# Kernel tuning notes

Measured on AMD Instinct MI355X. Metric: run time of the kernel, lower is better.

## Reference

```python
import jax, jax.numpy as jnp
import numpy as np

B, S, D = 4, 2048, 1024  # batch, seq_len, model dim (= qk_dim = output_dim)


def setup_inputs() -> dict:
    key = jax.random.key(0)
    kq, kk, kv, kwq, kwk, kwv = jax.random.split(key, 6)
    q = jax.random.normal(kq, (B, S, D), dtype=jnp.float32)
    k = jax.random.normal(kk, (B, S, D), dtype=jnp.float32)
    v = jax.random.normal(kv, (B, S, D), dtype=jnp.float32)
    # causal mask, broadcast over batch
    mask = jnp.broadcast_to(jnp.tril(jnp.ones((S, S), dtype=bool)), (B, S, S))
    W_q = jax.random.uniform(kwq, (D, D), dtype=jnp.float32)
    W_k = jax.random.uniform(kwk, (D, D), dtype=jnp.float32)
    W_v = jax.random.uniform(kwv, (D, D), dtype=jnp.float32)
    return {"q": q, "k": k, "v": v, "mask": mask, "W_q": W_q, "W_k": W_k, "W_v": W_v}


def reference(q, k, v, mask, W_q, W_k, W_v):
    q1 = q @ W_q  # (B, S, D)
    k1 = k @ W_k  # (B, S, D)
    v1 = v @ W_v  # (B, S, D)
    qk = jnp.einsum('bij,bkj->bik', q1, k1)  # (B, S, S)
    qk = qk * jax.lax.rsqrt(float(k1.shape[-1]))
    neg_inf = jnp.finfo(jnp.float32).min
    qk = jnp.where(mask, qk, neg_inf)
    s = jax.nn.softmax(qk, axis=-1)
    return jnp.einsum('bij,bjk->bik', s, v1)
```

## Files before the change

### kernel.cpp

```cpp
#include <hip/hip_runtime.h>
#include <hip/hip_bf16.h>
#include <float.h>


typedef __attribute__((ext_vector_type(8))) short bf16x8;
typedef __attribute__((ext_vector_type(4))) float f32x4;

#define MFMA16 __builtin_amdgcn_mfma_f32_16x16x32_bf16

union U8 { bf16x8 v; unsigned w[4]; };

__device__ __forceinline__ ushort f2bf(float x) {
  union { float f; unsigned u; } v; v.f = x;
  unsigned r = v.u + 0x7fffu + ((v.u >> 16) & 1u);
  return (ushort)(r >> 16);
}
__device__ __forceinline__ float bf2f(ushort h) {
  union { unsigned u; float f; } v; v.u = ((unsigned)h) << 16;
  return v.f;
}
__device__ __forceinline__ void splitf(float x, ushort& hi, ushort& lo) {
  hi = f2bf(x);
  lo = f2bf(x - bf2f(hi));
}

__device__ __forceinline__ bf16x8 cvt8(const float* lp) {
  U8 H;
#pragma unroll
  for (int p = 0; p < 4; ++p) {
    const unsigned u0 = __float_as_uint(lp[2 * p]);
    const unsigned u1 = __float_as_uint(lp[2 * p + 1]);
    const unsigned r0 = (u0 + 0x7fffu + ((u0 >> 16) & 1u)) >> 16;
    const unsigned r1 = (u1 + 0x7fffu + ((u1 >> 16) & 1u)) & 0xffff0000u;
    H.w[p] = r0 | r1;
  }
  return H.v;
}

#define GLOAD16(gp, lp)                                                        \
  __builtin_amdgcn_global_load_lds(                                            \
      (const __attribute__((address_space(1))) void*)(gp),                     \
      (__attribute__((address_space(3))) void*)(lp), 16, 0, 0)

__device__ __forceinline__ void stage_bf16_32(const ushort* g, int pitch,
                                              ushort* lds, int w, int lane) {
#pragma unroll
  for (int i = 0; i < 2; ++i) {
    const int c = w * 2 + i;
    const int row = c * 16 + (lane >> 2);
    const int kp = (lane & 3) * 8;
    GLOAD16(g + (size_t)row * pitch + kp, lds + c * 512);
  }
}
__device__ __forceinline__ void stage_bf16_64(const ushort* g, int pitch,
                                              ushort* lds, int w, int lane) {
#pragma unroll
  for (int i = 0; i < 4; ++i) {
    const int c = w * 4 + i;
    const int row = c * 8 + (lane >> 3);
    const int kp = (lane & 7) * 8;
    GLOAD16(g + (size_t)row * pitch + kp, lds + c * 512);
  }
}
__device__ __forceinline__ void stage_f32_32(const float* g, int pitch,
                                             float* lds, int w, int lane) {
#pragma unroll
  for (int i = 0; i < 4; ++i) {
    const int c = w * 4 + i;
    const int row = c * 8 + (lane >> 3);
    const int kp = (lane & 7) * 4;
    GLOAD16(g + (size_t)row * pitch + kp, lds + c * 256);
  }
}

__global__ __launch_bounds__(256) void split_pre(
    const float* __restrict__ q, const float* __restrict__ k,
    ushort* __restrict__ qh, ushort* __restrict__ ql,
    ushort* __restrict__ kh, ushort* __restrict__ kl) {
  const float* X = blockIdx.y ? k : q;
  ushort* H = blockIdx.y ? kh : qh;
  ushort* L = blockIdx.y ? kl : ql;
  const int n4 = 2097152;
  for (int i = blockIdx.x * 256 + threadIdx.x; i < n4; i += 2048 * 256) {
    const float4 x = reinterpret_cast<const float4*>(X)[i];
    ushort h0, l0, h1, l1, h2, l2, h3, l3;
    splitf(x.x, h0, l0); splitf(x.y, h1, l1);
    splitf(x.z, h2, l2); splitf(x.w, h3, l3);
    reinterpret_cast<ushort4*>(H)[i] = ushort4{h0, h1, h2, h3};
    reinterpret_cast<ushort4*>(L)[i] = ushort4{l0, l1, l2, l3};
  }
}

__global__ __launch_bounds__(256) void wt_conv(
    const float* __restrict__ W0, const float* __restrict__ W1,
    const float* __restrict__ W2, ushort* __restrict__ Th0,
    ushort* __restrict__ Tl0, ushort* __restrict__ Th1,
    ushort* __restrict__ Tl1, ushort* __restrict__ Th2) {
  __shared__ float t[32][33];
  const int z = blockIdx.z;
  const float* W = z == 0 ? W0 : (z == 1 ? W1 : W2);
  ushort* Th = z == 0 ? Th0 : (z == 1 ? Th1 : Th2);
  ushort* Tl = z == 0 ? Tl0 : (z == 1 ? Tl1 : nullptr);
  const int bx = blockIdx.x, by = blockIdx.y;
  const int r = threadIdx.x >> 3, c4 = (threadIdx.x & 7) * 4;
  const float4 x =
      *reinterpret_cast<const float4*>(&W[(size_t)(bx * 32 + r) * 1024 + by * 32 + c4]);
  t[r][c4] = x.x; t[r][c4 + 1] = x.y; t[r][c4 + 2] = x.z; t[r][c4 + 3] = x.w;
  __syncthreads();
  ushort h[4], l[4];
#pragma unroll
  for (int j = 0; j < 4; ++j) splitf(t[c4 + j][r], h[j], l[j]);
  const size_t o = (size_t)(by * 32 + r) * 1024 + bx * 32 + c4;
  *reinterpret_cast<ushort4*>(&Th[o]) = ushort4{h[0], h[1], h[2], h[3]};
  if (Tl)
    *reinterpret_cast<ushort4*>(&Tl[o]) = ushort4{l[0], l[1], l[2], l[3]};
}

__global__ __launch_bounds__(256) void proj_qk(
    const ushort* __restrict__ Ah0, const ushort* __restrict__ Al0,
    const ushort* __restrict__ Ah1, const ushort* __restrict__ Al1,
    const ushort* __restrict__ Bh0, const ushort* __restrict__ Bl0,
    const ushort* __restrict__ Bh1, const ushort* __restrict__ Bl1,
    ushort* __restrict__ Oh0, ushort* __restrict__ Ol0,
    ushort* __restrict__ Oh1, ushort* __restrict__ Ol1) {
  __shared__ ushort Ahs[4096], Als[4096], Bhs[4096], Bls[4096];
  const int f = blockIdx.x;
  const int xb = (f >> 3) & 7;
  const int r = (f & 7) + ((f >> 6) << 3);
  const int yb = r & 63, z = r >> 6;
  const ushort* Ah = z ? Ah1 : Ah0;
  const ushort* Al = z ? Al1 : Al0;
  const ushort* Bh = z ? Bh1 : Bh0;
  const ushort* Bl = z ? Bl1 : Bl0;
  ushort* Oh = z ? Oh1 : Oh0;
  ushort* Ol = z ? Ol1 : Ol0;
  const int tid = threadIdx.x, lane = tid & 63, w = tid >> 6;
  const int wr = w >> 1, wc = w & 1;
  const int lr = lane & 15, kg = lane >> 4;
  const int m0 = yb * 128, n0 = xb * 128;
  f32x4 acc[4][4] = {};

  for (int k0 = 0; k0 < 1024; k0 += 32) {
    stage_bf16_32(Ah + (size_t)m0 * 1024 + k0, 1024, Ahs, w, lane);
    stage_bf16_32(Al + (size_t)m0 * 1024 + k0, 1024, Als, w, lane);
    stage_bf16_32(Bh + (size_t)n0 * 1024 + k0, 1024, Bhs, w, lane);
    stage_bf16_32(Bl + (size_t)n0 * 1024 + k0, 1024, Bls, w, lane);
    __syncthreads();
    bf16x8 ah[4], al[4], bh[4], bl[4];
#pragma unroll
    for (int m = 0; m < 4; ++m) {
      ah[m] = *reinterpret_cast<bf16x8*>(&Ahs[(wr * 64 + m * 16 + lr) * 32 + kg * 8]);
      al[m] = *reinterpret_cast<bf16x8*>(&Als[(wr * 64 + m * 16 + lr) * 32 + kg * 8]);
    }
#pragma unroll
    for (int n = 0; n < 4; ++n) {
      bh[n] = *reinterpret_cast<bf16x8*>(&Bhs[(wc * 64 + n * 16 + lr) * 32 + kg * 8]);
      bl[n] = *reinterpret_cast<bf16x8*>(&Bls[(wc * 64 + n * 16 + lr) * 32 + kg * 8]);
    }
#pragma unroll
    for (int m = 0; m < 4; ++m)
#pragma unroll
      for (int n = 0; n < 4; ++n) {
        acc[m][n] = MFMA16(ah[m], bh[n], acc[m][n], 0, 0, 0);
        acc[m][n] = MFMA16(ah[m], bl[n], acc[m][n], 0, 0, 0);
        acc[m][n] = MFMA16(al[m], bh[n], acc[m][n], 0, 0, 0);
      }
    __syncthreads();
  }
#pragma unroll
  for (int m = 0; m < 4; ++m)
#pragma unroll
    for (int n = 0; n < 4; ++n)
#pragma unroll
      for (int reg = 0; reg < 4; ++reg) {
        const int gm = m0 + wr * 64 + m * 16 + kg * 4 + reg;
        const int gn = n0 + wc * 64 + n * 16 + lr;
        ushort h, l;
        splitf(acc[m][n][reg], h, l);
        Oh[(size_t)gm * 1024 + gn] = h;
        Ol[(size_t)gm * 1024 + gn] = l;
      }
}

__global__ __launch_bounds__(256) void proj_v(const ushort* __restrict__ Wvt,
                                              const float* __restrict__ V,
                                              ushort* __restrict__ v1t) {
  __shared__ ushort Ahs[4096];
  __shared__ float Bs[4096];
  const int f = blockIdx.x;
  const int yb = (f >> 3) & 7;
  const int xb = (f & 7) + ((f >> 6) << 3);
  const int tid = threadIdx.x, lane = tid & 63, w = tid >> 6;
  const int wr = w >> 1, wc = w & 1;
  const int lr = lane & 15, kg = lane >> 4;
  const int m0 = yb * 128;
  const int n0 = xb * 128;
  f32x4 acc[4][4] = {};

  for (int k0 = 0; k0 < 1024; k0 += 32) {
    stage_bf16_32(Wvt + (size_t)m0 * 1024 + k0, 1024, Ahs, w, lane);
    stage_f32_32(V + (size_t)n0 * 1024 + k0, 1024, Bs, w, lane);
    __syncthreads();
    bf16x8 ah[4], bh[4];
#pragma unroll
    for (int m = 0; m < 4; ++m)
      ah[m] = *reinterpret_cast<bf16x8*>(&Ahs[(wr * 64 + m * 16 + lr) * 32 + kg * 8]);
#pragma unroll
    for (int n = 0; n < 4; ++n)
      bh[n] = cvt8(&Bs[(wc * 64 + n * 16 + lr) * 32 + kg * 8]);
#pragma unroll
    for (int m = 0; m < 4; ++m)
#pragma unroll
      for (int n = 0; n < 4; ++n)
        acc[m][n] = MFMA16(ah[m], bh[n], acc[m][n], 0, 0, 0);
    __syncthreads();
  }
#pragma unroll
  for (int m = 0; m < 4; ++m)
#pragma unroll
    for (int n = 0; n < 4; ++n)
#pragma unroll
      for (int reg = 0; reg < 4; ++reg) {
        const int gm = m0 + wr * 64 + m * 16 + kg * 4 + reg;
        const int gn = n0 + wc * 64 + n * 16 + lr;
        const int b = gn >> 11, jj = gn & 2047;
        v1t[((size_t)b << 21) + (size_t)gm * 2048 + jj] = f2bf(acc[m][n][reg]);
      }
}

__global__ __launch_bounds__(256) void qk2(
    const ushort* __restrict__ q1h, const ushort* __restrict__ q1l,
    const ushort* __restrict__ k1h, const ushort* __restrict__ k1l,
    float* __restrict__ scoresA, float* __restrict__ scoresB) {
  __shared__ ushort Ahs[4096], Als[4096], Bhs[4096], Bls[4096];
  const int f = blockIdx.x;
  const int s = (f & 7) * 136 + (f >> 3);
  const int z = s / 544;
  const int rem = s % 544;
  const int b = rem / 136;
  int p = rem % 136, ti = 0, accp = 0;
  while (accp + ti + 1 <= p) { accp += ti + 1; ++ti; }
  const int tj = p - accp;
  const int tid = threadIdx.x, lane = tid & 63, w = tid >> 6;
  const int wr = w >> 1, wc = w & 1;
  const int lr = lane & 15, kg = lane >> 4;
  const int kh0 = z * 512;
  const ushort* qh = q1h + ((size_t)b * 2048 + ti * 128) * 1024 + kh0;
  const ushort* ql = q1l + ((size_t)b * 2048 + ti * 128) * 1024 + kh0;
  const ushort* kh = k1h + ((size_t)b * 2048 + tj * 128) * 1024 + kh0;
  const ushort* kl = k1l + ((size_t)b * 2048 + tj * 128) * 1024 + kh0;
  f32x4 acc[4][4] = {};

  for (int k0 = 0; k0 < 512; k0 += 32) {
    stage_bf16_32(qh + k0, 1024, Ahs, w, lane);
    stage_bf16_32(ql + k0, 1024, Als, w, lane);
    stage_bf16_32(kh + k0, 1024, Bhs, w, lane);
    stage_bf16_32(kl + k0, 1024, Bls, w, lane);
    __syncthreads();
    bf16x8 ah[4], al[4], bh[4], bl[4];
#pragma unroll
    for (int m = 0; m < 4; ++m) {
      ah[m] = *reinterpret_cast<bf16x8*>(&Ahs[(wr * 64 + m * 16 + lr) * 32 + kg * 8]);
      al[m] = *reinterpret_cast<bf16x8*>(&Als[(wr * 64 + m * 16 + lr) * 32 + kg * 8]);
    }
#pragma unroll
    for (int n = 0; n < 4; ++n) {
      bh[n] = *reinterpret_cast<bf16x8*>(&Bhs[(wc * 64 + n * 16 + lr) * 32 + kg * 8]);
      bl[n] = *reinterpret_cast<bf16x8*>(&Bls[(wc * 64 + n * 16 + lr) * 32 + kg * 8]);
    }
#pragma unroll
    for (int m = 0; m < 4; ++m)
#pragma unroll
      for (int n = 0; n < 4; ++n) {
        acc[m][n] = MFMA16(ah[m], bh[n], acc[m][n], 0, 0, 0);
        acc[m][n] = MFMA16(ah[m], bl[n], acc[m][n], 0, 0, 0);
        acc[m][n] = MFMA16(al[m], bh[n], acc[m][n], 0, 0, 0);
      }
    __syncthreads();
  }
  const float sc = 0.03125f;
  float* st = (z ? scoresB : scoresA) + ((size_t)b * 136 + p) * 16384;
#pragma unroll
  for (int m = 0; m < 4; ++m)
#pragma unroll
    for (int n = 0; n < 4; ++n)
#pragma unroll
      for (int reg = 0; reg < 4; ++reg) {
        const int il = wr * 64 + m * 16 + kg * 4 + reg;
        const int jl = wc * 64 + n * 16 + lr;
        st[il * 128 + jl] = acc[m][n][reg] * sc;
      }
}

__global__ __launch_bounds__(256) void softmax_kernel(
    float* __restrict__ scoresA, const float* __restrict__ scoresB) {
  __shared__ float red[8];
  const int rb = blockIdx.x;
  const int b = rb >> 11, r = rb & 2047;
  const int ti = r >> 7, rl = r & 127, ncol = (ti + 1) * 128;
  const int valid = r + 1;
  const size_t tbase = ((size_t)b * 136 + (ti * (ti + 1)) / 2) * 16384;
  float* srowA = scoresA + tbase;
  const float* srowB = scoresB + tbase;
  const int tid = threadIdx.x, lane = tid & 63, w = tid >> 6;

  float vals[2][4];
  float mx = -FLT_MAX;
#pragma unroll
  for (int c = 0; c < 2; ++c) {
    const int j = tid * 4 + c * 1024;
    const size_t o = (size_t)(j >> 7) * 16384 + rl * 128 + (j & 127);
    const float4 a = *reinterpret_cast<const float4*>(srowA + o);
    const float4 bb = *reinterpret_cast<const float4*>(srowB + o);
    vals[c][0] = (j + 0 < valid) ? a.x + bb.x : -FLT_MAX;
    vals[c][1] = (j + 1 < valid) ? a.y + bb.y : -FLT_MAX;
    vals[c][2] = (j + 2 < valid) ? a.z + bb.z : -FLT_MAX;
    vals[c][3] = (j + 3 < valid) ? a.w + bb.w : -FLT_MAX;
    mx = fmaxf(mx, fmaxf(fmaxf(vals[c][0], vals[c][1]),
                         fmaxf(vals[c][2], vals[c][3])));
  }
#pragma unroll
  for (int o = 32; o; o >>= 1) mx = fmaxf(mx, __shfl_xor(mx, o));
  if (lane == 0) red[w] = mx;
  __syncthreads();
  mx = fmaxf(fmaxf(red[0], red[1]), fmaxf(red[2], red[3]));

  float ex[2][4];
  float sum = 0.f;
#pragma unroll
  for (int c = 0; c < 2; ++c)
#pragma unroll
    for (int e = 0; e < 4; ++e) {
      const int j = tid * 4 + c * 1024 + e;
      ex[c][e] = (j < valid) ? __expf(vals[c][e] - mx) : 0.f;
      sum += ex[c][e];
    }
#pragma unroll
  for (int o = 32; o; o >>= 1) sum += __shfl_xor(sum, o);
  if (lane == 0) red[4 + w] = sum;
  __syncthreads();
  sum = red[4] + red[5] + red[6] + red[7];
  const float inv = 1.f / sum;
#pragma unroll
  for (int c = 0; c < 2; ++c) {
    const int j = tid * 4 + c * 1024;
    if (j < ncol) {
      ushort* pt = reinterpret_cast<ushort*>(srowA + (size_t)(j >> 7) * 16384);
      ushort4 pw;
      pw.x = f2bf(ex[c][0] * inv); pw.y = f2bf(ex[c][1] * inv);
      pw.z = f2bf(ex[c][2] * inv); pw.w = f2bf(ex[c][3] * inv);
      *reinterpret_cast<ushort4*>(&pt[rl * 256 + (j & 127)]) = pw;
    }
  }
}

__global__ __launch_bounds__(256) void pv2(const float* __restrict__ scores,
                                           const ushort* __restrict__ v1t,
                                           float* __restrict__ out) {
  __shared__ ushort Ps[128 * 64], Vs[128 * 64];
  const int fl = blockIdx.x;
  const int s = (fl & 7) * 64 + (fl >> 3);
  const int xb = s & 7, yb = (s >> 3) & 15, b = s >> 7;
  const int tid = threadIdx.x, lane = tid & 63, w = tid >> 6;
  const int wr = w >> 1, wc = w & 1;
  const int lr = lane & 15, kg = lane >> 4;
  const int ti = 15 - yb;
  const int n0 = xb * 128;
  const int tri_ti = (ti * (ti + 1)) / 2;
  const ushort* vbase = v1t + ((size_t)b << 21) + (size_t)n0 * 2048;
  const int kend = (ti + 1) * 128;
  f32x4 acc[4][4] = {};

  for (int k0 = 0; k0 < kend; k0 += 64) {
    const ushort* pt = reinterpret_cast<const ushort*>(
        scores + ((size_t)b * 136 + tri_ti + (k0 >> 7)) * 16384);
    stage_bf16_64(pt + (k0 & 64), 256, Ps, w, lane);
    stage_bf16_64(vbase + k0, 2048, Vs, w, lane);
    __syncthreads();
#pragma unroll
    for (int t2 = 0; t2 < 2; ++t2) {
      bf16x8 pa[4], vb[4];
#pragma unroll
      for (int m = 0; m < 4; ++m)
        pa[m] = *reinterpret_cast<bf16x8*>(
            &Ps[(wr * 64 + m * 16 + lr) * 64 + t2 * 32 + kg * 8]);
#pragma unroll
      for (int n = 0; n < 4; ++n)
        vb[n] = *reinterpret_cast<bf16x8*>(
            &Vs[(wc * 64 + n * 16 + lr) * 64 + t2 * 32 + kg * 8]);
#pragma unroll
      for (int m = 0; m < 4; ++m)
#pragma unroll
        for (int n = 0; n < 4; ++n)
          acc[m][n] = MFMA16(pa[m], vb[n], acc[m][n], 0, 0, 0);
    }
    __syncthreads();
  }
#pragma unroll
  for (int m = 0; m < 4; ++m)
#pragma unroll
    for (int n = 0; n < 4; ++n)
#pragma unroll
      for (int reg = 0; reg < 4; ++reg) {
        const int gm = ti * 128 + wr * 64 + m * 16 + kg * 4 + reg;
        const int gn = n0 + wc * 64 + n * 16 + lr;
        out[((size_t)b * 2048 + gm) * 1024 + gn] = acc[m][n][reg];
      }
}

extern "C" void kernel_launch(void* const* d_in, const int* in_sizes, int n_in,
                              void* d_out, int out_size, void* d_ws,
                              size_t ws_size, hipStream_t stream) {
  const float* q = (const float*)d_in[0];
  const float* k = (const float*)d_in[1];
  const float* v = (const float*)d_in[2];
  const float* Wq = (const float*)d_in[4];
  const float* Wk = (const float*)d_in[5];
  const float* Wv = (const float*)d_in[6];
  float* out = (float*)d_out;

  char* ws = (char*)d_ws;
  const size_t SCORES_T = 35651584;
  float* scoresA = (float*)ws;
  float* scoresB = (float*)(ws + SCORES_T);
  ushort* qsh = (ushort*)ws;
  ushort* qsl = qsh + 8388608;
  ushort* ksh = qsh + 2 * 8388608;
  ushort* ksl = qsh + 3 * 8388608;
  ushort* q1hi = (ushort*)(ws + 2 * SCORES_T);
  ushort* q1lo = q1hi + 8388608;
  ushort* k1hi = q1hi + 2 * 8388608;
  ushort* k1lo = q1hi + 3 * 8388608;
  ushort* v1t = (ushort*)(ws + 2 * SCORES_T);
  ushort* Wqth = (ushort*)(ws + 2 * SCORES_T + 67108864);
  ushort* Wqtl = Wqth + 1048576;
  ushort* Wkth = Wqth + 2097152;
  ushort* Wktl = Wqth + 3145728;
  ushort* Wvt  = Wqth + 4194304;
  const size_t need = 2 * SCORES_T + 67108864 + 10485760;
  if (ws_size < need) return;

  dim3 blk(256);
  wt_conv<<<dim3(32, 32, 3), blk, 0, stream>>>(Wq, Wk, Wv, Wqth, Wqtl, Wkth,
                                               Wktl, Wvt);
  split_pre<<<dim3(2048, 2), blk, 0, stream>>>(q, k, qsh, qsl, ksh, ksl);
  proj_qk<<<dim3(1024), blk, 0, stream>>>(qsh, qsl, ksh, ksl, Wqth, Wqtl,
                                          Wkth, Wktl, q1hi, q1lo, k1hi, k1lo);
  qk2<<<dim3(1088), blk, 0, stream>>>(q1hi, q1lo, k1hi, k1lo, scoresA,
                                      scoresB);
  softmax_kernel<<<dim3(8192), blk, 0, stream>>>(scoresA, scoresB);
  proj_v<<<dim3(512), blk, 0, stream>>>(Wvt, v, v1t);
  pv2<<<dim3(512), blk, 0, stream>>>(scoresA, v1t, out);
}
```

Before: 314.9 us.

## Merge independent launches into combined kernels and halve PV tile width

Weight transpose/split and the q/k split now run as branches of one kernel, and softmax and the V projection share one launch selected by block index. This removes two launches and lets independent work overlap on the GPU. The PV kernel now uses 128x64 output tiles instead of 128x128, doubling the block count to 1024 for better load balance over the causal triangle, at the cost of reloading the P tiles twice as often. Softmax blocks are now launched in the same grid as the MFMA-heavy projection blocks and must share shared-memory sizing with them, which can lower softmax occupancy.

```diff
diff --git a/kernel.cpp b/kernel.cpp
--- a/kernel.cpp
+++ b/kernel.cpp
@@ -62,6 +62,16 @@
     GLOAD16(g + (size_t)row * pitch + kp, lds + c * 512);
   }
 }
+__device__ __forceinline__ void stage_bf16_64x64(const ushort* g, int pitch,
+                                                 ushort* lds, int w, int lane) {
+#pragma unroll
+  for (int i = 0; i < 2; ++i) {
+    const int c = w * 2 + i;
+    const int row = c * 8 + (lane >> 3);
+    const int kp = (lane & 7) * 8;
+    GLOAD16(g + (size_t)row * pitch + kp, lds + c * 512);
+  }
+}
 __device__ __forceinline__ void stage_f32_32(const float* g, int pitch,
                                              float* lds, int w, int lane) {
 #pragma unroll
@@ -73,47 +83,49 @@
   }
 }
 
-__global__ __launch_bounds__(256) void split_pre(
+__global__ __launch_bounds__(256) void wt_split(
     const float* __restrict__ q, const float* __restrict__ k,
-    ushort* __restrict__ qh, ushort* __restrict__ ql,
-    ushort* __restrict__ kh, ushort* __restrict__ kl) {
-  const float* X = blockIdx.y ? k : q;
-  ushort* H = blockIdx.y ? kh : qh;
-  ushort* L = blockIdx.y ? kl : ql;
-  const int n4 = 2097152;
-  for (int i = blockIdx.x * 256 + threadIdx.x; i < n4; i += 2048 * 256) {
-    const float4 x = reinterpret_cast<const float4*>(X)[i];
-    ushort h0, l0, h1, l1, h2, l2, h3, l3;
-    splitf(x.x, h0, l0); splitf(x.y, h1, l1);
-    splitf(x.z, h2, l2); splitf(x.w, h3, l3);
-    reinterpret_cast<ushort4*>(H)[i] = ushort4{h0, h1, h2, h3};
-    reinterpret_cast<ushort4*>(L)[i] = ushort4{l0, l1, l2, l3};
-  }
-}
-
-__global__ __launch_bounds__(256) void wt_conv(
     const float* __restrict__ W0, const float* __restrict__ W1,
     const float* __restrict__ W2, ushort* __restrict__ Th0,
     ushort* __restrict__ Tl0, ushort* __restrict__ Th1,
-    ushort* __restrict__ Tl1, ushort* __restrict__ Th2) {
+    ushort* __restrict__ Tl1, ushort* __restrict__ Th2,
+    ushort* __restrict__ qh, ushort* __restrict__ ql,
+    ushort* __restrict__ kh, ushort* __restrict__ kl) {
   __shared__ float t[32][33];
-  const int z = blockIdx.z;
-  const float* W = z == 0 ? W0 : (z == 1 ? W1 : W2);
-  ushort* Th = z == 0 ? Th0 : (z == 1 ? Th1 : Th2);
-  ushort* Tl = z == 0 ? Tl0 : (z == 1 ? Tl1 : nullptr);
-  const int bx = blockIdx.x, by = blockIdx.y;
-  const int r = threadIdx.x >> 3, c4 = (threadIdx.x & 7) * 4;
-  const float4 x =
-      *reinterpret_cast<const float4*>(&W[(size_t)(bx * 32 + r) * 1024 + by * 32 + c4]);
-  t[r][c4] = x.x; t[r][c4 + 1] = x.y; t[r][c4 + 2] = x.z; t[r][c4 + 3] = x.w;
-  __syncthreads();
-  ushort h[4], l[4];
-#pragma unroll
-  for (int j = 0; j < 4; ++j) splitf(t[c4 + j][r], h[j], l[j]);
-  const size_t o = (size_t)(by * 32 + r) * 1024 + bx * 32 + c4;
-  *reinterpret_cast<ushort4*>(&Th[o]) = ushort4{h[0], h[1], h[2], h[3]};
-  if (Tl)
-    *reinterpret_cast<ushort4*>(&Tl[o]) = ushort4{l[0], l[1], l[2], l[3]};
+  const int f = blockIdx.x;
+  if (f < 3072) {
+    const int z = f >> 10, r10 = f & 1023;
+    const int bx = r10 & 31, by = r10 >> 5;
+    const float* W = z == 0 ? W0 : (z == 1 ? W1 : W2);
+    ushort* Th = z == 0 ? Th0 : (z == 1 ? Th1 : Th2);
+    ushort* Tl = z == 0 ? Tl0 : (z == 1 ? Tl1 : nullptr);
+    const int r = threadIdx.x >> 3, c4 = (threadIdx.x & 7) * 4;
+    const float4 x = *reinterpret_cast<const float4*>(
+        &W[(size_t)(bx * 32 + r) * 1024 + by * 32 + c4]);
+    t[r][c4] = x.x; t[r][c4 + 1] = x.y; t[r][c4 + 2] = x.z; t[r][c4 + 3] = x.w;
+    __syncthreads();
+    ushort h[4], l[4];
+#pragma unroll
+    for (int j = 0; j < 4; ++j) splitf(t[c4 + j][r], h[j], l[j]);
+    const size_t o = (size_t)(by * 32 + r) * 1024 + bx * 32 + c4;
+    *reinterpret_cast<ushort4*>(&Th[o]) = ushort4{h[0], h[1], h[2], h[3]};
+    if (Tl)
+      *reinterpret_cast<ushort4*>(&Tl[o]) = ushort4{l[0], l[1], l[2], l[3]};
+  } else {
+    const int fl = f - 3072;
+    const float* X = (fl >> 11) ? k : q;
+    ushort* H = (fl >> 11) ? kh : qh;
+    ushort* L = (fl >> 11) ? kl : ql;
+    const int n4 = 2097152;
+    for (int i = (fl & 2047) * 256 + threadIdx.x; i < n4; i += 2048 * 256) {
+      const float4 x = reinterpret_cast<const float4*>(X)[i];
+      ushort h0, l0, h1, l1, h2, l2, h3, l3;
+      splitf(x.x, h0, l0); splitf(x.y, h1, l1);
+      splitf(x.z, h2, l2); splitf(x.w, h3, l3);
+      reinterpret_cast<ushort4*>(H)[i] = ushort4{h0, h1, h2, h3};
+      reinterpret_cast<ushort4*>(L)[i] = ushort4{l0, l1, l2, l3};
+    }
+  }
 }
 
 __global__ __launch_bounds__(256) void proj_qk(
@@ -182,52 +194,6 @@
       }
 }
 
-__global__ __launch_bounds__(256) void proj_v(const ushort* __restrict__ Wvt,
-                                              const float* __restrict__ V,
-                                              ushort* __restrict__ v1t) {
-  __shared__ ushort Ahs[4096];
-  __shared__ float Bs[4096];
-  const int f = blockIdx.x;
-  const int yb = (f >> 3) & 7;
-  const int xb = (f & 7) + ((f >> 6) << 3);
-  const int tid = threadIdx.x, lane = tid & 63, w = tid >> 6;
-  const int wr = w >> 1, wc = w & 1;
-  const int lr = lane & 15, kg = lane >> 4;
-  const int m0 = yb * 128;
-  const int n0 = xb * 128;
-  f32x4 acc[4][4] = {};
-
-  for (int k0 = 0; k0 < 1024; k0 += 32) {
-    stage_bf16_32(Wvt + (size_t)m0 * 1024 + k0, 1024, Ahs, w, lane);
-    stage_f32_32(V + (size_t)n0 * 1024 + k0, 1024, Bs, w, lane);
-    __syncthreads();
-    bf16x8 ah[4], bh[4];
-#pragma unroll
-    for (int m = 0; m < 4; ++m)
-      ah[m] = *reinterpret_cast<bf16x8*>(&Ahs[(wr * 64 + m * 16 + lr) * 32 + kg * 8]);
-#pragma unroll
-    for (int n = 0; n < 4; ++n)
-      bh[n] = cvt8(&Bs[(wc * 64 + n * 16 + lr) * 32 + kg * 8]);
-#pragma unroll
-    for (int m = 0; m < 4; ++m)
-#pragma unroll
-      for (int n = 0; n < 4; ++n)
-        acc[m][n] = MFMA16(ah[m], bh[n], acc[m][n], 0, 0, 0);
-    __syncthreads();
-  }
-#pragma unroll
-  for (int m = 0; m < 4; ++m)
-#pragma unroll
-    for (int n = 0; n < 4; ++n)
-#pragma unroll
-      for (int reg = 0; reg < 4; ++reg) {
-        const int gm = m0 + wr * 64 + m * 16 + kg * 4 + reg;
-        const int gn = n0 + wc * 64 + n * 16 + lr;
-        const int b = gn >> 11, jj = gn & 2047;
-        v1t[((size_t)b << 21) + (size_t)gm * 2048 + jj] = f2bf(acc[m][n][reg]);
-      }
-}
-
 __global__ __launch_bounds__(256) void qk2(
     const ushort* __restrict__ q1h, const ushort* __restrict__ q1l,
     const ushort* __restrict__ k1h, const ushort* __restrict__ k1l,
@@ -292,106 +258,154 @@
       }
 }
 
-__global__ __launch_bounds__(256) void softmax_kernel(
-    float* __restrict__ scoresA, const float* __restrict__ scoresB) {
-  __shared__ float red[8];
-  const int rb = blockIdx.x;
-  const int b = rb >> 11, r = rb & 2047;
-  const int ti = r >> 7, rl = r & 127, ncol = (ti + 1) * 128;
-  const int valid = r + 1;
-  const size_t tbase = ((size_t)b * 136 + (ti * (ti + 1)) / 2) * 16384;
-  float* srowA = scoresA + tbase;
-  const float* srowB = scoresB + tbase;
+__global__ __launch_bounds__(256) void sm_projv(
+    float* __restrict__ scoresA, const float* __restrict__ scoresB,
+    const ushort* __restrict__ Wvt, const float* __restrict__ V,
+    ushort* __restrict__ v1t) {
+  __shared__ __align__(16) char smem[24576];
   const int tid = threadIdx.x, lane = tid & 63, w = tid >> 6;
-
-  float vals[2][4];
-  float mx = -FLT_MAX;
-#pragma unroll
-  for (int c = 0; c < 2; ++c) {
-    const int j = tid * 4 + c * 1024;
-    const size_t o = (size_t)(j >> 7) * 16384 + rl * 128 + (j & 127);
-    const float4 a = *reinterpret_cast<const float4*>(srowA + o);
-    const float4 bb = *reinterpret_cast<const float4*>(srowB + o);
-    vals[c][0] = (j + 0 < valid) ? a.x + bb.x : -FLT_MAX;
-    vals[c][1] = (j + 1 < valid) ? a.y + bb.y : -FLT_MAX;
-    vals[c][2] = (j + 2 < valid) ? a.z + bb.z : -FLT_MAX;
-    vals[c][3] = (j + 3 < valid) ? a.w + bb.w : -FLT_MAX;
-    mx = fmaxf(mx, fmaxf(fmaxf(vals[c][0], vals[c][1]),
-                         fmaxf(vals[c][2], vals[c][3])));
-  }
-#pragma unroll
-  for (int o = 32; o; o >>= 1) mx = fmaxf(mx, __shfl_xor(mx, o));
-  if (lane == 0) red[w] = mx;
-  __syncthreads();
-  mx = fmaxf(fmaxf(red[0], red[1]), fmaxf(red[2], red[3]));
-
-  float ex[2][4];
-  float sum = 0.f;
-#pragma unroll
-  for (int c = 0; c < 2; ++c)
-#pragma unroll
-    for (int e = 0; e < 4; ++e) {
-      const int j = tid * 4 + c * 1024 + e;
-      ex[c][e] = (j < valid) ? __expf(vals[c][e] - mx) : 0.f;
-      sum += ex[c][e];
-    }
-#pragma unroll
-  for (int o = 32; o; o >>= 1) sum += __shfl_xor(sum, o);
-  if (lane == 0) red[4 + w] = sum;
-  __syncthreads();
-  sum = red[4] + red[5] + red[6] + red[7];
-  const float inv = 1.f / sum;
-#pragma unroll
-  for (int c = 0; c < 2; ++c) {
-    const int j = tid * 4 + c * 1024;
-    if (j < ncol) {
-      ushort* pt = reinterpret_cast<ushort*>(srowA + (size_t)(j >> 7) * 16384);
-      ushort4 pw;
-      pw.x = f2bf(ex[c][0] * inv); pw.y = f2bf(ex[c][1] * inv);
-      pw.z = f2bf(ex[c][2] * inv); pw.w = f2bf(ex[c][3] * inv);
-      *reinterpret_cast<ushort4*>(&pt[rl * 256 + (j & 127)]) = pw;
-    }
+  const int fg = blockIdx.x;
+  if (fg < 8192) {
+    float* red = reinterpret_cast<float*>(smem);
+    const int b = fg >> 11, r = fg & 2047;
+    const int ti = r >> 7, rl = r & 127, ncol = (ti + 1) * 128;
+    const int valid = r + 1;
+    const size_t tbase = ((size_t)b * 136 + (ti * (ti + 1)) / 2) * 16384;
+    float* srowA = scoresA + tbase;
+    const float* srowB = scoresB + tbase;
+
+    float vals[2][4];
+    float mx = -FLT_MAX;
+#pragma unroll
+    for (int c = 0; c < 2; ++c) {
+      const int j = tid * 4 + c * 1024;
+      const size_t o = (size_t)(j >> 7) * 16384 + rl * 128 + (j & 127);
+      const float4 a = *reinterpret_cast<const float4*>(srowA + o);
+      const float4 bb = *reinterpret_cast<const float4*>(srowB + o);
+      vals[c][0] = (j + 0 < valid) ? a.x + bb.x : -FLT_MAX;
+      vals[c][1] = (j + 1 < valid) ? a.y + bb.y : -FLT_MAX;
+      vals[c][2] = (j + 2 < valid) ? a.z + bb.z : -FLT_MAX;
+      vals[c][3] = (j + 3 < valid) ? a.w + bb.w : -FLT_MAX;
+      mx = fmaxf(mx, fmaxf(fmaxf(vals[c][0], vals[c][1]),
+                           fmaxf(vals[c][2], vals[c][3])));
+    }
+#pragma unroll
+    for (int o = 32; o; o >>= 1) mx = fmaxf(mx, __shfl_xor(mx, o));
+    if (lane == 0) red[w] = mx;
+    __syncthreads();
+    mx = fmaxf(fmaxf(red[0], red[1]), fmaxf(red[2], red[3]));
+
+    float ex[2][4];
+    float sum = 0.f;
+#pragma unroll
+    for (int c = 0; c < 2; ++c)
+#pragma unroll
+      for (int e = 0; e < 4; ++e) {
+        const int j = tid * 4 + c * 1024 + e;
+        ex[c][e] = (j < valid) ? __expf(vals[c][e] - mx) : 0.f;
+        sum += ex[c][e];
+      }
+#pragma unroll
+    for (int o = 32; o; o >>= 1) sum += __shfl_xor(sum, o);
+    if (lane == 0) red[4 + w] = sum;
+    __syncthreads();
+    sum = red[4] + red[5] + red[6] + red[7];
+    const float inv = 1.f / sum;
+#pragma unroll
+    for (int c = 0; c < 2; ++c) {
+      const int j = tid * 4 + c * 1024;
+      if (j < ncol) {
+        ushort* pt =
+            reinterpret_cast<ushort*>(srowA + (size_t)(j >> 7) * 16384);
+        ushort4 pw;
+        pw.x = f2bf(ex[c][0] * inv); pw.y = f2bf(ex[c][1] * inv);
+        pw.z = f2bf(ex[c][2] * inv); pw.w = f2bf(ex[c][3] * inv);
+        *reinterpret_cast<ushort4*>(&pt[rl * 256 + (j & 127)]) = pw;
+      }
+    }
+  } else {
+    ushort* Ahs = reinterpret_cast<ushort*>(smem);
+    float* Bs = reinterpret_cast<float*>(smem + 8192);
+    const int f2 = fg - 8192;
+    const int yb = (f2 >> 3) & 7;
+    const int xb = (f2 & 7) + ((f2 >> 6) << 3);
+    const int wr = w >> 1, wc = w & 1;
+    const int lr = lane & 15, kg = lane >> 4;
+    const int m0 = yb * 128;
+    const int n0 = xb * 128;
+    f32x4 acc[4][4] = {};
+
+    for (int k0 = 0; k0 < 1024; k0 += 32) {
+      stage_bf16_32(Wvt + (size_t)m0 * 1024 + k0, 1024, Ahs, w, lane);
+      stage_f32_32(V + (size_t)n0 * 1024 + k0, 1024, Bs, w, lane);
+      __syncthreads();
+      bf16x8 ah[4], bh[4];
+#pragma unroll
+      for (int m = 0; m < 4; ++m)
+        ah[m] = *reinterpret_cast<bf16x8*>(
+            &Ahs[(wr * 64 + m * 16 + lr) * 32 + kg * 8]);
+#pragma unroll
+      for (int n = 0; n < 4; ++n)
+        bh[n] = cvt8(&Bs[(wc * 64 + n * 16 + lr) * 32 + kg * 8]);
+#pragma unroll
+      for (int m = 0; m < 4; ++m)
+#pragma unroll
+        for (int n = 0; n < 4; ++n)
+          acc[m][n] = MFMA16(ah[m], bh[n], acc[m][n], 0, 0, 0);
+      __syncthreads();
+    }
+#pragma unroll
+    for (int m = 0; m < 4; ++m)
+#pragma unroll
+      for (int n = 0; n < 4; ++n)
+#pragma unroll
+        for (int reg = 0; reg < 4; ++reg) {
+          const int gm = m0 + wr * 64 + m * 16 + kg * 4 + reg;
+          const int gn = n0 + wc * 64 + n * 16 + lr;
+          const int b = gn >> 11, jj = gn & 2047;
+          v1t[((size_t)b << 21) + (size_t)gm * 2048 + jj] = f2bf(acc[m][n][reg]);
+        }
   }
 }
 
 __global__ __launch_bounds__(256) void pv2(const float* __restrict__ scores,
                                            const ushort* __restrict__ v1t,
                                            float* __restrict__ out) {
-  __shared__ ushort Ps[128 * 64], Vs[128 * 64];
+  __shared__ ushort Ps[128 * 64], Vs[64 * 64];
   const int fl = blockIdx.x;
-  const int s = (fl & 7) * 64 + (fl >> 3);
-  const int xb = s & 7, yb = (s >> 3) & 15, b = s >> 7;
+  const int s = (fl & 7) * 128 + (fl >> 3);
+  const int b = s >> 8, rem = s & 255;
+  const int ti = 15 - (rem >> 4);
+  const int n0 = (rem & 15) * 64;
   const int tid = threadIdx.x, lane = tid & 63, w = tid >> 6;
   const int wr = w >> 1, wc = w & 1;
   const int lr = lane & 15, kg = lane >> 4;
-  const int ti = 15 - yb;
-  const int n0 = xb * 128;
   const int tri_ti = (ti * (ti + 1)) / 2;
   const ushort* vbase = v1t + ((size_t)b << 21) + (size_t)n0 * 2048;
   const int kend = (ti + 1) * 128;
-  f32x4 acc[4][4] = {};
+  f32x4 acc[4][2] = {};
 
   for (int k0 = 0; k0 < kend; k0 += 64) {
     const ushort* pt = reinterpret_cast<const ushort*>(
         scores + ((size_t)b * 136 + tri_ti + (k0 >> 7)) * 16384);
     stage_bf16_64(pt + (k0 & 64), 256, Ps, w, lane);
-    stage_bf16_64(vbase + k0, 2048, Vs, w, lane);
+    stage_bf16_64x64(vbase + k0, 2048, Vs, w, lane);
     __syncthreads();
 #pragma unroll
     for (int t2 = 0; t2 < 2; ++t2) {
-      bf16x8 pa[4], vb[4];
+      bf16x8 pa[4], vb[2];
 #pragma unroll
       for (int m = 0; m < 4; ++m)
         pa[m] = *reinterpret_cast<bf16x8*>(
             &Ps[(wr * 64 + m * 16 + lr) * 64 + t2 * 32 + kg * 8]);
 #pragma unroll
-      for (int n = 0; n < 4; ++n)
+      for (int n = 0; n < 2; ++n)
         vb[n] = *reinterpret_cast<bf16x8*>(
-            &Vs[(wc * 64 + n * 16 + lr) * 64 + t2 * 32 + kg * 8]);
+            &Vs[(wc * 32 + n * 16 + lr) * 64 + t2 * 32 + kg * 8]);
 #pragma unroll
       for (int m = 0; m < 4; ++m)
 #pragma unroll
-        for (int n = 0; n < 4; ++n)
+        for (int n = 0; n < 2; ++n)
           acc[m][n] = MFMA16(pa[m], vb[n], acc[m][n], 0, 0, 0);
     }
     __syncthreads();
@@ -399,11 +413,11 @@
 #pragma unroll
   for (int m = 0; m < 4; ++m)
 #pragma unroll
-    for (int n = 0; n < 4; ++n)
+    for (int n = 0; n < 2; ++n)
 #pragma unroll
       for (int reg = 0; reg < 4; ++reg) {
         const int gm = ti * 128 + wr * 64 + m * 16 + kg * 4 + reg;
-        const int gn = n0 + wc * 64 + n * 16 + lr;
+        const int gn = n0 + wc * 32 + n * 16 + lr;
         out[((size_t)b * 2048 + gm) * 1024 + gn] = acc[m][n][reg];
       }
 }
@@ -441,14 +455,12 @@
   if (ws_size < need) return;
 
   dim3 blk(256);
-  wt_conv<<<dim3(32, 32, 3), blk, 0, stream>>>(Wq, Wk, Wv, Wqth, Wqtl, Wkth,
-                                               Wktl, Wvt);
-  split_pre<<<dim3(2048, 2), blk, 0, stream>>>(q, k, qsh, qsl, ksh, ksl);
+  wt_split<<<dim3(7168), blk, 0, stream>>>(q, k, Wq, Wk, Wv, Wqth, Wqtl, Wkth,
+                                           Wktl, Wvt, qsh, qsl, ksh, ksl);
   proj_qk<<<dim3(1024), blk, 0, stream>>>(qsh, qsl, ksh, ksl, Wqth, Wqtl,
                                           Wkth, Wktl, q1hi, q1lo, k1hi, k1lo);
   qk2<<<dim3(1088), blk, 0, stream>>>(q1hi, q1lo, k1hi, k1lo, scoresA,
                                       scoresB);
-  softmax_kernel<<<dim3(8192), blk, 0, stream>>>(scoresA, scoresB);
-  proj_v<<<dim3(512), blk, 0, stream>>>(Wvt, v, v1t);
-  pv2<<<dim3(512), blk, 0, stream>>>(scoresA, v1t, out);
-}
+  sm_projv<<<dim3(8704), blk, 0, stream>>>(scoresA, scoresB, Wvt, v, v1t);
+  pv2<<<dim3(1024), blk, 0, stream>>>(scoresA, v1t, out);
+}
```

Measured after the change: 312.6 us. Within noise of the previous version (-0.7%).
